# Kernel optimization log

Measured on AMD Instinct MI355X. Metric: run time of the kernel, lower is better.

Reference implementation:

```python
import jax, jax.numpy as jnp
import numpy as np
import math

DIM = 256
D_STATE = 16
D_CONV = 4
EXPAND = 2
D_INNER = EXPAND * DIM
DT_RANK = math.ceil(DIM / 16)
B_, H_, W_ = 2, 48, 48


def setup_inputs() -> dict:
    key = jax.random.key(0)
    ks = jax.random.split(key, 13)
    s = lambda *sh: 1.0 / np.sqrt(sh[-1])
    inp = {
        "x": jax.random.normal(ks[0], (B_, DIM, H_, W_), jnp.float32),
        "ln_w": jnp.ones((DIM,), jnp.float32),
        "ln_b": jnp.zeros((DIM,), jnp.float32),
        "in_proj_w": jax.random.normal(ks[1], (2 * D_INNER, DIM), jnp.float32) * s(DIM),
        "conv_w": jax.random.normal(ks[2], (D_INNER, 1, D_CONV), jnp.float32) * s(D_CONV),
        "conv_b": jax.random.normal(ks[3], (D_INNER,), jnp.float32) * 0.1,
        "x_proj_w": jax.random.normal(ks[4], (DT_RANK + 2 * D_STATE, D_INNER), jnp.float32) * s(D_INNER),
        "dt_proj_w": jax.random.normal(ks[5], (D_INNER, DT_RANK), jnp.float32) * s(DT_RANK),
        "dt_proj_b": jax.random.uniform(ks[6], (D_INNER,), jnp.float32, -4.0, -1.0),  # softplus -> small dt
        "A_log": jnp.log(jnp.broadcast_to(jnp.arange(1, D_STATE + 1, dtype=jnp.float32), (D_INNER, D_STATE))),
        "D": jnp.ones((D_INNER,), jnp.float32),
        "out_proj_w": jax.random.normal(ks[7], (DIM, D_INNER), jnp.float32) * s(D_INNER),
        "gamma": jax.random.normal(ks[8], (1,), jnp.float32) * 0.1,
    }
    return inp


def _mamba(seq, in_proj_w, conv_w, conv_b, x_proj_w, dt_proj_w, dt_proj_b, A_log, D, out_proj_w):
    # seq: [B, L, dim]
    B, L, _ = seq.shape
    xz = seq @ in_proj_w.T                       # [B, L, 2*d_inner]
    x_in, z = jnp.split(xz, 2, axis=-1)
    # depthwise causal conv over time
    xt = jnp.transpose(x_in, (0, 2, 1))          # [B, d_inner, L]
    xc = jax.lax.conv_general_dilated(
        xt, conv_w, window_strides=(1,), padding=[(D_CONV - 1, 0)],
        feature_group_count=D_INNER, dimension_numbers=("NCH", "OIH", "NCH"))
    xc = xc + conv_b[None, :, None]
    xc = jax.nn.silu(xc)
    xu = jnp.transpose(xc, (0, 2, 1))            # [B, L, d_inner]
    # input-dependent SSM params
    x_dbl = xu @ x_proj_w.T                      # [B, L, dt_rank + 2N]
    dt, Bm, Cm = jnp.split(x_dbl, [DT_RANK, DT_RANK + D_STATE], axis=-1)
    delta = jax.nn.softplus(dt @ dt_proj_w.T + dt_proj_b)   # [B, L, d_inner]
    A = -jnp.exp(A_log)                          # [d_inner, N]
    dA = jnp.exp(delta[..., None] * A)           # [B, L, d_inner, N]
    dBx = (delta * xu)[..., None] * Bm[:, :, None, :]        # [B, L, d_inner, N]

    def step(h, ins):
        dA_t, dBx_t, C_t = ins
        h = dA_t * h + dBx_t                     # [B, d_inner, N]
        y = jnp.einsum("bdn,bn->bd", h, C_t)
        return h, y

    h0 = jnp.zeros((B, D_INNER, D_STATE), seq.dtype)
    xs = (jnp.swapaxes(dA, 0, 1), jnp.swapaxes(dBx, 0, 1), jnp.swapaxes(Cm, 0, 1))
    _, ys = jax.lax.scan(step, h0, xs)           # ys: [L, B, d_inner]
    y = jnp.swapaxes(ys, 0, 1) + xu * D          # [B, L, d_inner]
    y = y * jax.nn.silu(z)
    return y @ out_proj_w.T                      # [B, L, dim]


def reference(x, ln_w, ln_b, in_proj_w, conv_w, conv_b, x_proj_w, dt_proj_w,
              dt_proj_b, A_log, D, out_proj_w, gamma):
    B, C, H, W = x.shape
    shortcut = x
    xp = jnp.transpose(x, (0, 2, 3, 1))          # [B, H, W, C]
    mu = jnp.mean(xp, axis=-1, keepdims=True)
    var = jnp.var(xp, axis=-1, keepdims=True)
    xn = (xp - mu) * jax.lax.rsqrt(var + 1e-5) * ln_w + ln_b
    seq = xn.reshape(B, H * W, C)
    y = _mamba(seq, in_proj_w, conv_w, conv_b, x_proj_w, dt_proj_w, dt_proj_b,
               A_log, D, out_proj_w)
    y = jnp.transpose(y.reshape(B, H, W, C), (0, 3, 1, 2))
    return shortcut + gamma * y
```

## Files before the change

### kernel.cpp

```cpp
#include <hip/hip_runtime.h>
#include <math.h>

#define DIMC 256
#define DST 16
#define DIN 512
#define BB 2
#define HH 48
#define WW 48
#define LL (HH*WW)
#define MM (BB*LL)
#define CH 12
#define NC 192
#define NGRP (BB*DIN)
#define NSEQ (NGRP*DST)
#define LTILE 16

typedef unsigned short ushort_t;
typedef __attribute__((ext_vector_type(8))) short bf16x8;
typedef __attribute__((ext_vector_type(4))) float f32x4;

__device__ __forceinline__ float silu_f(float a){ return a / (1.f + expf(-a)); }
__device__ __forceinline__ float softplus_f(float a){ return a > 20.f ? a : log1pf(__expf(a)); }
__device__ __forceinline__ ushort_t f2bf(float f) {
    unsigned u = __float_as_uint(f);
    u += 0x7FFFu + ((u >> 16) & 1u);
    return (ushort_t)(u >> 16);
}
__device__ __forceinline__ float bf2f(ushort_t h) {
    return __uint_as_float(((unsigned)h) << 16);
}

__global__ __launch_bounds__(256) void ln_kernel(const float* __restrict__ x,
    const float* __restrict__ w, const float* __restrict__ bgain,
    ushort_t* __restrict__ xn) {
    __shared__ float T2[LTILE][DIMC + 4];
    __shared__ float PS[16][17], PS2[16][17];
    __shared__ float MUB[LTILE], RB[LTILE];
    int blk = blockIdx.x;
    int b = blk / (LL/LTILE);
    int l0 = (blk % (LL/LTILE)) * LTILE;
    int t = threadIdx.x;
    int p = t & 15, g = t >> 4;
    float v[16];
    float s = 0.f, s2 = 0.f;
    #pragma unroll
    for (int cc = 0; cc < 16; cc++) {
        int c = g*16 + cc;
        float vv = x[((size_t)(b*DIMC + c))*LL + l0 + p];
        v[cc] = vv;
        s += vv; s2 += vv*vv;
    }
    PS[g][p] = s; PS2[g][p] = s2;
    __syncthreads();
    if (t < 16) {
        float tot = 0.f, tot2 = 0.f;
        #pragma unroll
        for (int gg = 0; gg < 16; gg++) { tot += PS[gg][t]; tot2 += PS2[gg][t]; }
        float mu = tot * (1.f/DIMC);
        float var = tot2 * (1.f/DIMC) - mu*mu;
        MUB[t] = mu;
        RB[t] = rsqrtf(var + 1e-5f);
    }
    __syncthreads();
    float mu = MUB[p], r = RB[p];
    #pragma unroll
    for (int cc = 0; cc < 16; cc++) {
        int c = g*16 + cc;
        T2[p][c] = (v[cc] - mu) * r * w[c] + bgain[c];
    }
    __syncthreads();
    int c4 = (t & 63) * 4;
    int prow = t >> 6;
    #pragma unroll
    for (int pp = 0; pp < 4; pp++) {
        int pos = pp*4 + prow;
        float4 q = *(const float4*)&T2[pos][c4];
        ushort4 o;
        o.x = f2bf(q.x); o.y = f2bf(q.y); o.z = f2bf(q.z); o.w = f2bf(q.w);
        *(ushort4*)&xn[((size_t)(b*LL + l0 + pos))*DIMC + c4] = o;
    }
}

#define W0N (1024*256)
#define W1N (48*512)
#define W2N (256*512)
__global__ __launch_bounds__(256) void wsetup_kernel(const float* __restrict__ w0,
    const float* __restrict__ w1, const float* __restrict__ w2,
    const float* __restrict__ A_log,
    ushort_t* __restrict__ o0, ushort_t* __restrict__ o1, ushort_t* __restrict__ o2,
    float* __restrict__ A2) {
    int i = blockIdx.x * 256 + threadIdx.x;
    if (i < W0N) o0[i] = f2bf(w0[i]);
    else if (i < W0N + W1N) o1[i - W0N] = f2bf(w1[i - W0N]);
    else if (i < W0N + W1N + W2N) o2[i - W0N - W1N] = f2bf(w2[i - W0N - W1N]);
    if (i < DIN*DST) A2[i] = -__expf(A_log[i]);
}

__global__ __launch_bounds__(256) void mfma_gemm128_split(const ushort_t* __restrict__ A,
    const ushort_t* __restrict__ W, ushort_t* __restrict__ Xs, float* __restrict__ Zb,
    int K) {
    __shared__ ushort_t Asl[128][72];
    __shared__ ushort_t Bsl[128][72];
    int tid = threadIdx.x;
    int bm = blockIdx.y * 128;
    int bn = blockIdx.x * 128;
    int w = tid >> 6, l = tid & 63;
    int wr = (w >> 1) * 64, wc = (w & 1) * 64;
    int fr = l & 15, fg = l >> 4;
    f32x4 acc[4][4] = {};
    for (int k0 = 0; k0 < K; k0 += 64) {
        #pragma unroll
        for (int s = 0; s < 4; s++) {
            int c = tid + s*256;
            int r = c >> 3, c8 = (c & 7) * 8;
            *(uint4*)&Asl[r][c8] = *(const uint4*)(A + (size_t)(bm + r)*K + k0 + c8);
            *(uint4*)&Bsl[r][c8] = *(const uint4*)(W + (size_t)(bn + r)*K + k0 + c8);
        }
        __syncthreads();
        #pragma unroll
        for (int kk = 0; kk < 2; kk++) {
            int ko = kk*32 + fg*8;
            bf16x8 af[4], bf[4];
            #pragma unroll
            for (int i = 0; i < 4; i++) af[i] = *(const bf16x8*)&Asl[wr + i*16 + fr][ko];
            #pragma unroll
            for (int j = 0; j < 4; j++) bf[j] = *(const bf16x8*)&Bsl[wc + j*16 + fr][ko];
            #pragma unroll
            for (int i = 0; i < 4; i++)
                #pragma unroll
                for (int j = 0; j < 4; j++)
                    acc[i][j] = __builtin_amdgcn_mfma_f32_16x16x32_bf16(af[i], bf[j], acc[i][j], 0,0,0);
        }
        __syncthreads();
    }
    #pragma unroll
    for (int i = 0; i < 4; i++)
        #pragma unroll
        for (int j = 0; j < 4; j++) {
            int n = bn + wc + j*16 + fr;
            int mbase = bm + wr + i*16 + fg*4;
            if (n < DIN) {
                #pragma unroll
                for (int ii = 0; ii < 4; ii++)
                    Xs[(size_t)(mbase+ii)*DIN + n] = f2bf(acc[i][j][ii]);
            } else {
                #pragma unroll
                for (int ii = 0; ii < 4; ii++)
                    Zb[(size_t)(mbase+ii)*DIN + (n - DIN)] = acc[i][j][ii];
            }
        }
}

template<int EPI>
__global__ __launch_bounds__(256) void mfma_gemm(const ushort_t* __restrict__ A,
    const ushort_t* __restrict__ W, float* __restrict__ C, int M, int N, int K,
    const float* __restrict__ Xres, const float* __restrict__ gammap,
    float* __restrict__ Out) {
    __shared__ ushort_t Asl[64][72];
    __shared__ ushort_t Bsl[64][72];
    int tid = threadIdx.x;
    int bm = blockIdx.y * 64;
    int bn = blockIdx.x * 64;
    int w = tid >> 6, l = tid & 63;
    int wr = (w >> 1) * 32, wc = (w & 1) * 32;
    int fr = l & 15, fg = l >> 4;
    f32x4 acc[2][2] = {};
    for (int k0 = 0; k0 < K; k0 += 64) {
        #pragma unroll
        for (int s = 0; s < 2; s++) {
            int c = tid + s*256;
            int r = c >> 3, c8 = (c & 7) * 8;
            *(uint4*)&Asl[r][c8] = *(const uint4*)(A + (size_t)(bm + r)*K + k0 + c8);
            uint4 wv = make_uint4(0u,0u,0u,0u);
            if (bn + r < N) wv = *(const uint4*)(W + (size_t)(bn + r)*K + k0 + c8);
            *(uint4*)&Bsl[r][c8] = wv;
        }
        __syncthreads();
        #pragma unroll
        for (int kk = 0; kk < 2; kk++) {
            int ko = kk*32 + fg*8;
            bf16x8 a0 = *(const bf16x8*)&Asl[wr + fr][ko];
            bf16x8 a1 = *(const bf16x8*)&Asl[wr + 16 + fr][ko];
            bf16x8 b0 = *(const bf16x8*)&Bsl[wc + fr][ko];
            bf16x8 b1 = *(const bf16x8*)&Bsl[wc + 16 + fr][ko];
            acc[0][0] = __builtin_amdgcn_mfma_f32_16x16x32_bf16(a0, b0, acc[0][0], 0,0,0);
            acc[0][1] = __builtin_amdgcn_mfma_f32_16x16x32_bf16(a0, b1, acc[0][1], 0,0,0);
            acc[1][0] = __builtin_amdgcn_mfma_f32_16x16x32_bf16(a1, b0, acc[1][0], 0,0,0);
            acc[1][1] = __builtin_amdgcn_mfma_f32_16x16x32_bf16(a1, b1, acc[1][1], 0,0,0);
        }
        __syncthreads();
    }
    if (EPI == 0) {
        #pragma unroll
        for (int mi = 0; mi < 2; mi++)
            #pragma unroll
            for (int nj = 0; nj < 2; nj++) {
                int n = bn + wc + nj*16 + fr;
                if (n < N) {
                    int mbase = bm + wr + mi*16 + fg*4;
                    #pragma unroll
                    for (int i = 0; i < 4; i++)
                        C[(size_t)(mbase + i)*N + n] = acc[mi][nj][i];
                }
            }
    } else {
        float g = gammap[0];
        int b = (bm >= LL) ? 1 : 0;
        #pragma unroll
        for (int mi = 0; mi < 2; mi++)
            #pragma unroll
            for (int nj = 0; nj < 2; nj++) {
                int n = bn + wc + nj*16 + fr;
                int mbase = bm + wr + mi*16 + fg*4;
                #pragma unroll
                for (int i = 0; i < 4; i++) {
                    size_t o = ((size_t)(b*DIMC + n))*LL + (size_t)(mbase + i - b*LL);
                    Out[o] = fmaf(g, acc[mi][nj][i], Xres[o]);
                }
            }
    }
}

__global__ __launch_bounds__(256) void conv_kernel(const ushort_t* __restrict__ xs,
    const float* __restrict__ cw, const float* __restrict__ cb,
    ushort_t* __restrict__ xu) {
    int idx = blockIdx.x * 256 + threadIdx.x;
    int d = idx & (DIN-1);
    int ml = idx >> 9;
    int l = ml % LL;
    float acc = cb[d];
    #pragma unroll
    for (int j = 0; j < 4; j++) {
        int ll = l - 3 + j;
        if (ll >= 0) acc = fmaf(cw[d*4 + j], bf2f(xs[(size_t)(ml - l + ll)*DIN + d]), acc);
    }
    xu[(size_t)ml*DIN + d] = f2bf(silu_f(acc));
}

#define LOAD16(arr, p) { float4 q0=(p)[0],q1=(p)[1],q2=(p)[2],q3=(p)[3]; \
    arr[0]=q0.x;arr[1]=q0.y;arr[2]=q0.z;arr[3]=q0.w; arr[4]=q1.x;arr[5]=q1.y;arr[6]=q1.z;arr[7]=q1.w; \
    arr[8]=q2.x;arr[9]=q2.y;arr[10]=q2.z;arr[11]=q2.w; arr[12]=q3.x;arr[13]=q3.y;arr[14]=q3.z;arr[15]=q3.w; }

#define DT_DOT(dlt, xr) { float4 t0 = (xr)[0], t1 = (xr)[1], t2 = (xr)[2], t3 = (xr)[3]; \
    dlt=fmaf(t0.x,dw[0],dlt); dlt=fmaf(t0.y,dw[1],dlt); dlt=fmaf(t0.z,dw[2],dlt); dlt=fmaf(t0.w,dw[3],dlt); \
    dlt=fmaf(t1.x,dw[4],dlt); dlt=fmaf(t1.y,dw[5],dlt); dlt=fmaf(t1.z,dw[6],dlt); dlt=fmaf(t1.w,dw[7],dlt); \
    dlt=fmaf(t2.x,dw[8],dlt); dlt=fmaf(t2.y,dw[9],dlt); dlt=fmaf(t2.z,dw[10],dlt); dlt=fmaf(t2.w,dw[11],dlt); \
    dlt=fmaf(t3.x,dw[12],dlt); dlt=fmaf(t3.y,dw[13],dlt); dlt=fmaf(t3.z,dw[14],dlt); dlt=fmaf(t3.w,dw[15],dlt); }

__global__ __launch_bounds__(256) void scan_phase1(
    const ushort_t* __restrict__ xu, const float* __restrict__ xdbl,
    const float* __restrict__ dtw, const float* __restrict__ dtb,
    const float* __restrict__ A2,
    float* __restrict__ aprod, float* __restrict__ hend) {
    __shared__ float xs_s[CH*48];
    int t = blockIdx.x * 256 + threadIdx.x;
    int g = t & (NGRP-1);
    int c = t >> 10;
    int b = g >> 9, d = g & (DIN-1);
    int m0 = b*LL + c*CH;
    for (int i = threadIdx.x; i < CH*48; i += 256) xs_s[i] = xdbl[(size_t)m0*48 + i];
    float dw[16], A[16], h[16], a[16];
    LOAD16(dw, (const float4*)(dtw + (size_t)d*16));
    LOAD16(A,  (const float4*)(A2  + (size_t)d*16));
    #pragma unroll
    for (int n = 0; n < 16; n++) { h[n] = 0.f; a[n] = 1.f; }
    float bias = dtb[d];
    __syncthreads();
    for (int l = 0; l < CH; l++) {
        const float4* xr = (const float4*)&xs_s[l*48];
        float dlt = bias;
        DT_DOT(dlt, xr);
        dlt = softplus_f(dlt);
        float xv = bf2f(xu[(size_t)(m0 + l)*DIN + d]);
        float dbx = dlt * xv;
        float Bv[16];
        LOAD16(Bv, xr + 4);
        #pragma unroll
        for (int n = 0; n < 16; n++) {
            float dA = __expf(dlt * A[n]);
            h[n] = fmaf(dA, h[n], dbx * Bv[n]);
            a[n] *= dA;
        }
    }
    float4* ap = (float4*)(aprod + ((size_t)c*NGRP + g)*16);
    float4* hp = (float4*)(hend  + ((size_t)c*NGRP + g)*16);
    ap[0] = make_float4(a[0],a[1],a[2],a[3]);   ap[1] = make_float4(a[4],a[5],a[6],a[7]);
    ap[2] = make_float4(a[8],a[9],a[10],a[11]); ap[3] = make_float4(a[12],a[13],a[14],a[15]);
    hp[0] = make_float4(h[0],h[1],h[2],h[3]);   hp[1] = make_float4(h[4],h[5],h[6],h[7]);
    hp[2] = make_float4(h[8],h[9],h[10],h[11]); hp[3] = make_float4(h[12],h[13],h[14],h[15]);
}

__global__ __launch_bounds__(256) void scan_phase2(const float* __restrict__ aprod,
    const float* __restrict__ hend, float* __restrict__ hin) {
    int u = blockIdx.x * 256 + threadIdx.x;
    float h = 0.f;
    #pragma unroll 4
    for (int c = 0; c < NC; c++) {
        size_t ci = (size_t)c*NSEQ + u;
        hin[ci] = h;
        h = fmaf(aprod[ci], h, hend[ci]);
    }
}

__global__ __launch_bounds__(256) void scan_phase3(
    const ushort_t* __restrict__ xu, const float* __restrict__ xdbl,
    const float* __restrict__ dtw, const float* __restrict__ dtb,
    const float* __restrict__ A2, const float* __restrict__ Dp,
    const float* __restrict__ zbuf, const float* __restrict__ hin,
    ushort_t* __restrict__ yg) {
    __shared__ float xs_s[CH*48];
    int t = blockIdx.x * 256 + threadIdx.x;
    int g = t & (NGRP-1);
    int c = t >> 10;
    int b = g >> 9, d = g & (DIN-1);
    int m0 = b*LL + c*CH;
    for (int i = threadIdx.x; i < CH*48; i += 256) xs_s[i] = xdbl[(size_t)m0*48 + i];
    float dw[16], A[16], h[16];
    LOAD16(dw, (const float4*)(dtw + (size_t)d*16));
    LOAD16(A,  (const float4*)(A2  + (size_t)d*16));
    LOAD16(h,  (const float4*)(hin + ((size_t)c*NGRP + g)*16));
    float bias = dtb[d];
    float Dd = Dp[d];
    __syncthreads();
    for (int l = 0; l < CH; l++) {
        int m = m0 + l;
        const float4* xr = (const float4*)&xs_s[l*48];
        float dlt = bias;
        DT_DOT(dlt, xr);
        dlt = softplus_f(dlt);
        float xv = bf2f(xu[(size_t)m*DIN + d]);
        float dbx = dlt * xv;
        float Bv[16], Cv[16];
        LOAD16(Bv, xr + 4);
        LOAD16(Cv, xr + 8);
        float y = 0.f;
        #pragma unroll
        for (int n = 0; n < 16; n++) {
            float dA = __expf(dlt * A[n]);
            h[n] = fmaf(dA, h[n], dbx * Bv[n]);
            y = fmaf(h[n], Cv[n], y);
        }
        float z = zbuf[(size_t)m*DIN + d];
        float yv = fmaf(xv, Dd, y);
        yg[(size_t)m*DIN + d] = f2bf(yv * (z / (1.f + __expf(-z))));
    }
}

extern "C" void kernel_launch(void* const* d_in, const int* in_sizes, int n_in,
                              void* d_out, int out_size, void* d_ws, size_t ws_size,
                              hipStream_t stream) {
    const float* x         = (const float*)d_in[0];
    const float* ln_w      = (const float*)d_in[1];
    const float* ln_b      = (const float*)d_in[2];
    const float* in_proj_w = (const float*)d_in[3];
    const float* conv_w    = (const float*)d_in[4];
    const float* conv_b    = (const float*)d_in[5];
    const float* x_proj_w  = (const float*)d_in[6];
    const float* dt_proj_w = (const float*)d_in[7];
    const float* dt_proj_b = (const float*)d_in[8];
    const float* A_log     = (const float*)d_in[9];
    const float* Dp        = (const float*)d_in[10];
    const float* out_proj_w= (const float*)d_in[11];
    const float* gamma     = (const float*)d_in[12];
    float* out = (float*)d_out;

    float* ws = (float*)d_ws;
    float* zbuf  = ws;
    float* x_dbl = zbuf  + (size_t)MM*DIN;
    float* aprod = x_dbl + (size_t)MM*48;
    float* hend  = aprod + (size_t)NC*NSEQ;
    float* hin   = hend  + (size_t)NC*NSEQ;
    float* A2    = hin   + (size_t)NC*NSEQ;
    ushort_t* xn  = (ushort_t*)(A2 + DIN*DST);
    ushort_t* xs  = xn  + (size_t)MM*DIMC;
    ushort_t* xu  = xs  + (size_t)MM*DIN;
    ushort_t* yg  = xu  + (size_t)MM*DIN;
    ushort_t* win = yg  + (size_t)MM*DIN;
    ushort_t* wxp = win + (size_t)W0N;
    ushort_t* wout= wxp + (size_t)W1N;

    ln_kernel<<<BB*(LL/LTILE), 256, 0, stream>>>(x, ln_w, ln_b, xn);
    wsetup_kernel<<<(W0N+W1N+W2N+255)/256, 256, 0, stream>>>(in_proj_w, x_proj_w, out_proj_w, A_log, win, wxp, wout, A2);
    mfma_gemm128_split<<<dim3(1024/128, MM/128), 256, 0, stream>>>(xn, win, xs, zbuf, DIMC);
    conv_kernel<<<(MM*DIN)/256, 256, 0, stream>>>(xs, conv_w, conv_b, xu);
    mfma_gemm<0><<<dim3(1, MM/64), 256, 0, stream>>>(xu, wxp, x_dbl, MM, 48, DIN, nullptr, nullptr, nullptr);
    scan_phase1<<<(NC*NGRP)/256, 256, 0, stream>>>(xu, x_dbl, dt_proj_w, dt_proj_b, A2, aprod, hend);
    scan_phase2<<<NSEQ/256, 256, 0, stream>>>(aprod, hend, hin);
    scan_phase3<<<(NC*NGRP)/256, 256, 0, stream>>>(xu, x_dbl, dt_proj_w, dt_proj_b, A2, Dp, zbuf, hin, yg);
    mfma_gemm<2><<<dim3(DIMC/64, MM/64), 256, 0, stream>>>(yg, wout, nullptr, MM, DIMC, DIN, x, gamma, out);
}
```

Baseline: 202.5 us.

## Fuse conv into x_proj GEMM, merge LN with weight setup, store z as bf16

Merges the layernorm and weight-conversion kernels into one launch. The depthwise causal conv plus SiLU now runs inside the x_proj GEMM tile loader, so a separate conv kernel is gone. The z half of in_proj is stored as bf16 instead of fp32, halving its write and read traffic. The cost is recomputing 3 halo rows per tile and some extra rounding on z. It also saves two kernel launches.

```diff
diff --git a/kernel.cpp b/kernel.cpp
--- a/kernel.cpp
+++ b/kernel.cpp
@@ -14,6 +14,11 @@
 #define NGRP (BB*DIN)
 #define NSEQ (NGRP*DST)
 #define LTILE 16
+#define NBLN (BB*(LL/LTILE))
+#define W0N (1024*256)
+#define W1N (48*512)
+#define W2N (256*512)
+#define NBW  ((W0N+W1N+W2N)/256)
 
 typedef unsigned short ushort_t;
 typedef __attribute__((ext_vector_type(8))) short bf16x8;
@@ -30,16 +35,27 @@
     return __uint_as_float(((unsigned)h) << 16);
 }
 
-__global__ __launch_bounds__(256) void ln_kernel(const float* __restrict__ x,
-    const float* __restrict__ w, const float* __restrict__ bgain,
-    ushort_t* __restrict__ xn) {
+__global__ __launch_bounds__(256) void prep_kernel(const float* __restrict__ x,
+    const float* __restrict__ w, const float* __restrict__ bgain, ushort_t* __restrict__ xn,
+    const float* __restrict__ w0, const float* __restrict__ w1, const float* __restrict__ w2,
+    const float* __restrict__ A_log,
+    ushort_t* __restrict__ o0, ushort_t* __restrict__ o1, ushort_t* __restrict__ o2,
+    float* __restrict__ A2) {
     __shared__ float T2[LTILE][DIMC + 4];
     __shared__ float PS[16][17], PS2[16][17];
     __shared__ float MUB[LTILE], RB[LTILE];
     int blk = blockIdx.x;
+    int t = threadIdx.x;
+    if (blk >= NBLN) {
+        int i = (blk - NBLN) * 256 + t;
+        if (i < W0N) o0[i] = f2bf(w0[i]);
+        else if (i < W0N + W1N) o1[i - W0N] = f2bf(w1[i - W0N]);
+        else o2[i - W0N - W1N] = f2bf(w2[i - W0N - W1N]);
+        if (i < DIN*DST) A2[i] = -__expf(A_log[i]);
+        return;
+    }
     int b = blk / (LL/LTILE);
     int l0 = (blk % (LL/LTILE)) * LTILE;
-    int t = threadIdx.x;
     int p = t & 15, g = t >> 4;
     float v[16];
     float s = 0.f, s2 = 0.f;
@@ -81,23 +97,8 @@
     }
 }
 
-#define W0N (1024*256)
-#define W1N (48*512)
-#define W2N (256*512)
-__global__ __launch_bounds__(256) void wsetup_kernel(const float* __restrict__ w0,
-    const float* __restrict__ w1, const float* __restrict__ w2,
-    const float* __restrict__ A_log,
-    ushort_t* __restrict__ o0, ushort_t* __restrict__ o1, ushort_t* __restrict__ o2,
-    float* __restrict__ A2) {
-    int i = blockIdx.x * 256 + threadIdx.x;
-    if (i < W0N) o0[i] = f2bf(w0[i]);
-    else if (i < W0N + W1N) o1[i - W0N] = f2bf(w1[i - W0N]);
-    else if (i < W0N + W1N + W2N) o2[i - W0N - W1N] = f2bf(w2[i - W0N - W1N]);
-    if (i < DIN*DST) A2[i] = -__expf(A_log[i]);
-}
-
 __global__ __launch_bounds__(256) void mfma_gemm128_split(const ushort_t* __restrict__ A,
-    const ushort_t* __restrict__ W, ushort_t* __restrict__ Xs, float* __restrict__ Zb,
+    const ushort_t* __restrict__ W, ushort_t* __restrict__ Xs, ushort_t* __restrict__ Zb,
     int K) {
     __shared__ ushort_t Asl[128][72];
     __shared__ ushort_t Bsl[128][72];
@@ -120,16 +121,16 @@
         #pragma unroll
         for (int kk = 0; kk < 2; kk++) {
             int ko = kk*32 + fg*8;
-            bf16x8 af[4], bf[4];
+            bf16x8 af[4], bfm[4];
             #pragma unroll
             for (int i = 0; i < 4; i++) af[i] = *(const bf16x8*)&Asl[wr + i*16 + fr][ko];
             #pragma unroll
-            for (int j = 0; j < 4; j++) bf[j] = *(const bf16x8*)&Bsl[wc + j*16 + fr][ko];
+            for (int j = 0; j < 4; j++) bfm[j] = *(const bf16x8*)&Bsl[wc + j*16 + fr][ko];
             #pragma unroll
             for (int i = 0; i < 4; i++)
                 #pragma unroll
                 for (int j = 0; j < 4; j++)
-                    acc[i][j] = __builtin_amdgcn_mfma_f32_16x16x32_bf16(af[i], bf[j], acc[i][j], 0,0,0);
+                    acc[i][j] = __builtin_amdgcn_mfma_f32_16x16x32_bf16(af[i], bfm[j], acc[i][j], 0,0,0);
         }
         __syncthreads();
     }
@@ -146,7 +147,84 @@
             } else {
                 #pragma unroll
                 for (int ii = 0; ii < 4; ii++)
-                    Zb[(size_t)(mbase+ii)*DIN + (n - DIN)] = acc[i][j][ii];
+                    Zb[(size_t)(mbase+ii)*DIN + (n - DIN)] = f2bf(acc[i][j][ii]);
+            }
+        }
+}
+
+__global__ __launch_bounds__(256) void xproj_conv_kernel(
+    const ushort_t* __restrict__ xs, const ushort_t* __restrict__ wxp,
+    const float* __restrict__ cw, const float* __restrict__ cb,
+    ushort_t* __restrict__ xu, float* __restrict__ xdbl) {
+    __shared__ ushort_t Xt[67][72];
+    __shared__ ushort_t As[64][72];
+    __shared__ ushort_t Bs[64][72];
+    int tid = threadIdx.x;
+    int R0 = blockIdx.x * 64;
+    int lmin = (R0 >= LL) ? LL : 0;
+    int w = tid >> 6, l = tid & 63;
+    int wr = (w >> 1) * 32, wc = (w & 1) * 32;
+    int fr = l & 15, fg = l >> 4;
+    f32x4 acc[2][2] = {};
+    for (int k0 = 0; k0 < DIN; k0 += 64) {
+        for (int i = tid; i < 67*8; i += 256) {
+            int r = i >> 3, c8 = (i & 7) * 8;
+            int m = R0 - 3 + r;
+            uint4 v = make_uint4(0u,0u,0u,0u);
+            if (m >= lmin) v = *(const uint4*)(xs + (size_t)m*DIN + k0 + c8);
+            *(uint4*)&Xt[r][c8] = v;
+        }
+        for (int i = tid; i < 64*8; i += 256) {
+            int r = i >> 3, c8 = (i & 7) * 8;
+            uint4 v = make_uint4(0u,0u,0u,0u);
+            if (r < 48) v = *(const uint4*)(wxp + (size_t)r*DIN + k0 + c8);
+            *(uint4*)&Bs[r][c8] = v;
+        }
+        __syncthreads();
+        #pragma unroll
+        for (int rr = 0; rr < 2; rr++) {
+            int r = (tid >> 3) + rr*32;
+            int c0 = (tid & 7) * 8;
+            ushort_t ov[8];
+            #pragma unroll
+            for (int cc = 0; cc < 8; cc++) {
+                int c = c0 + cc;
+                float4 cwv = ((const float4*)cw)[k0 + c];
+                float a = cb[k0 + c];
+                a = fmaf(cwv.x, bf2f(Xt[r+0][c]), a);
+                a = fmaf(cwv.y, bf2f(Xt[r+1][c]), a);
+                a = fmaf(cwv.z, bf2f(Xt[r+2][c]), a);
+                a = fmaf(cwv.w, bf2f(Xt[r+3][c]), a);
+                ov[cc] = f2bf(silu_f(a));
+            }
+            *(uint4*)&As[r][c0] = *(uint4*)ov;
+            *(uint4*)(xu + (size_t)(R0 + r)*DIN + k0 + c0) = *(uint4*)ov;
+        }
+        __syncthreads();
+        #pragma unroll
+        for (int kk = 0; kk < 2; kk++) {
+            int ko = kk*32 + fg*8;
+            bf16x8 a0 = *(const bf16x8*)&As[wr + fr][ko];
+            bf16x8 a1 = *(const bf16x8*)&As[wr + 16 + fr][ko];
+            bf16x8 b0 = *(const bf16x8*)&Bs[wc + fr][ko];
+            bf16x8 b1 = *(const bf16x8*)&Bs[wc + 16 + fr][ko];
+            acc[0][0] = __builtin_amdgcn_mfma_f32_16x16x32_bf16(a0, b0, acc[0][0], 0,0,0);
+            acc[0][1] = __builtin_amdgcn_mfma_f32_16x16x32_bf16(a0, b1, acc[0][1], 0,0,0);
+            acc[1][0] = __builtin_amdgcn_mfma_f32_16x16x32_bf16(a1, b0, acc[1][0], 0,0,0);
+            acc[1][1] = __builtin_amdgcn_mfma_f32_16x16x32_bf16(a1, b1, acc[1][1], 0,0,0);
+        }
+        __syncthreads();
+    }
+    #pragma unroll
+    for (int mi = 0; mi < 2; mi++)
+        #pragma unroll
+        for (int nj = 0; nj < 2; nj++) {
+            int n = wc + nj*16 + fr;
+            if (n < 48) {
+                int mbase = R0 + wr + mi*16 + fg*4;
+                #pragma unroll
+                for (int i = 0; i < 4; i++)
+                    xdbl[(size_t)(mbase + i)*48 + n] = acc[mi][nj][i];
             }
         }
 }
@@ -221,22 +299,6 @@
     }
 }
 
-__global__ __launch_bounds__(256) void conv_kernel(const ushort_t* __restrict__ xs,
-    const float* __restrict__ cw, const float* __restrict__ cb,
-    ushort_t* __restrict__ xu) {
-    int idx = blockIdx.x * 256 + threadIdx.x;
-    int d = idx & (DIN-1);
-    int ml = idx >> 9;
-    int l = ml % LL;
-    float acc = cb[d];
-    #pragma unroll
-    for (int j = 0; j < 4; j++) {
-        int ll = l - 3 + j;
-        if (ll >= 0) acc = fmaf(cw[d*4 + j], bf2f(xs[(size_t)(ml - l + ll)*DIN + d]), acc);
-    }
-    xu[(size_t)ml*DIN + d] = f2bf(silu_f(acc));
-}
-
 #define LOAD16(arr, p) { float4 q0=(p)[0],q1=(p)[1],q2=(p)[2],q3=(p)[3]; \
     arr[0]=q0.x;arr[1]=q0.y;arr[2]=q0.z;arr[3]=q0.w; arr[4]=q1.x;arr[5]=q1.y;arr[6]=q1.z;arr[7]=q1.w; \
     arr[8]=q2.x;arr[9]=q2.y;arr[10]=q2.z;arr[11]=q2.w; arr[12]=q3.x;arr[13]=q3.y;arr[14]=q3.z;arr[15]=q3.w; }
@@ -306,7 +368,7 @@
     const ushort_t* __restrict__ xu, const float* __restrict__ xdbl,
     const float* __restrict__ dtw, const float* __restrict__ dtb,
     const float* __restrict__ A2, const float* __restrict__ Dp,
-    const float* __restrict__ zbuf, const float* __restrict__ hin,
+    const ushort_t* __restrict__ zb, const float* __restrict__ hin,
     ushort_t* __restrict__ yg) {
     __shared__ float xs_s[CH*48];
     int t = blockIdx.x * 256 + threadIdx.x;
@@ -340,7 +402,7 @@
             h[n] = fmaf(dA, h[n], dbx * Bv[n]);
             y = fmaf(h[n], Cv[n], y);
         }
-        float z = zbuf[(size_t)m*DIN + d];
+        float z = bf2f(zb[(size_t)m*DIN + d]);
         float yv = fmaf(xv, Dd, y);
         yg[(size_t)m*DIN + d] = f2bf(yv * (z / (1.f + __expf(-z))));
     }
@@ -365,27 +427,26 @@
     float* out = (float*)d_out;
 
     float* ws = (float*)d_ws;
-    float* zbuf  = ws;
-    float* x_dbl = zbuf  + (size_t)MM*DIN;
+    float* x_dbl = ws;
     float* aprod = x_dbl + (size_t)MM*48;
     float* hend  = aprod + (size_t)NC*NSEQ;
     float* hin   = hend  + (size_t)NC*NSEQ;
     float* A2    = hin   + (size_t)NC*NSEQ;
     ushort_t* xn  = (ushort_t*)(A2 + DIN*DST);
     ushort_t* xs  = xn  + (size_t)MM*DIMC;
-    ushort_t* xu  = xs  + (size_t)MM*DIN;
+    ushort_t* zb  = xs  + (size_t)MM*DIN;
+    ushort_t* xu  = zb  + (size_t)MM*DIN;
     ushort_t* yg  = xu  + (size_t)MM*DIN;
     ushort_t* win = yg  + (size_t)MM*DIN;
     ushort_t* wxp = win + (size_t)W0N;
     ushort_t* wout= wxp + (size_t)W1N;
 
-    ln_kernel<<<BB*(LL/LTILE), 256, 0, stream>>>(x, ln_w, ln_b, xn);
-    wsetup_kernel<<<(W0N+W1N+W2N+255)/256, 256, 0, stream>>>(in_proj_w, x_proj_w, out_proj_w, A_log, win, wxp, wout, A2);
-    mfma_gemm128_split<<<dim3(1024/128, MM/128), 256, 0, stream>>>(xn, win, xs, zbuf, DIMC);
-    conv_kernel<<<(MM*DIN)/256, 256, 0, stream>>>(xs, conv_w, conv_b, xu);
-    mfma_gemm<0><<<dim3(1, MM/64), 256, 0, stream>>>(xu, wxp, x_dbl, MM, 48, DIN, nullptr, nullptr, nullptr);
+    prep_kernel<<<NBLN + NBW, 256, 0, stream>>>(x, ln_w, ln_b, xn,
+        in_proj_w, x_proj_w, out_proj_w, A_log, win, wxp, wout, A2);
+    mfma_gemm128_split<<<dim3(1024/128, MM/128), 256, 0, stream>>>(xn, win, xs, zb, DIMC);
+    xproj_conv_kernel<<<MM/64, 256, 0, stream>>>(xs, wxp, conv_w, conv_b, xu, x_dbl);
     scan_phase1<<<(NC*NGRP)/256, 256, 0, stream>>>(xu, x_dbl, dt_proj_w, dt_proj_b, A2, aprod, hend);
     scan_phase2<<<NSEQ/256, 256, 0, stream>>>(aprod, hend, hin);
-    scan_phase3<<<(NC*NGRP)/256, 256, 0, stream>>>(xu, x_dbl, dt_proj_w, dt_proj_b, A2, Dp, zbuf, hin, yg);
+    scan_phase3<<<(NC*NGRP)/256, 256, 0, stream>>>(xu, x_dbl, dt_proj_w, dt_proj_b, A2, Dp, zb, hin, yg);
     mfma_gemm<2><<<dim3(DIMC/64, MM/64), 256, 0, stream>>>(yg, wout, nullptr, MM, DIMC, DIN, x, gamma, out);
 }
```

Result: slower. 209.4 us (+3.4%).

## Fuse scan phases into a cooperative kernel, merge prep kernels, store z in bf16

Applied to the files above, without the earlier changes.

Three scan kernels become one cooperative kernel that uses two grid-wide syncs in place of separate launches, and it keeps the phase-1 registers alive into phase 3. The chunk length is doubled, so there are half as many chunks. Layernorm and weight conversion are merged into one prep kernel that converts with float4 loads, and the z gate buffer is stored as bf16 instead of fp32 to cut memory traffic. The cooperative launch needs all 384 blocks resident at once. The serial cross-chunk scan uses only NSEQ threads while the rest of the grid waits, and bf16 z adds rounding error.

```diff
diff --git a/kernel.cpp b/kernel.cpp
--- a/kernel.cpp
+++ b/kernel.cpp
@@ -1,5 +1,8 @@
 #include <hip/hip_runtime.h>
+#include <hip/hip_cooperative_groups.h>
 #include <math.h>
+
+namespace cg = cooperative_groups;
 
 #define DIMC 256
 #define DST 16
@@ -9,11 +12,16 @@
 #define WW 48
 #define LL (HH*WW)
 #define MM (BB*LL)
-#define CH 12
-#define NC 192
+#define CH 24
+#define NC 96
 #define NGRP (BB*DIN)
 #define NSEQ (NGRP*DST)
 #define LTILE 16
+#define NBLN (BB*(LL/LTILE))
+#define W0N (1024*256)
+#define W1N (48*512)
+#define W2N (256*512)
+#define NB4  ((W0N+W1N+W2N)/4/256)
 
 typedef unsigned short ushort_t;
 typedef __attribute__((ext_vector_type(8))) short bf16x8;
@@ -30,16 +38,36 @@
     return __uint_as_float(((unsigned)h) << 16);
 }
 
-__global__ __launch_bounds__(256) void ln_kernel(const float* __restrict__ x,
-    const float* __restrict__ w, const float* __restrict__ bgain,
-    ushort_t* __restrict__ xn) {
+__global__ __launch_bounds__(256) void prep_kernel(const float* __restrict__ x,
+    const float* __restrict__ w, const float* __restrict__ bgain, ushort_t* __restrict__ xn,
+    const float* __restrict__ w0, const float* __restrict__ w1, const float* __restrict__ w2,
+    const float* __restrict__ A_log,
+    ushort_t* __restrict__ o0, ushort_t* __restrict__ o1, ushort_t* __restrict__ o2,
+    float* __restrict__ A2) {
     __shared__ float T2[LTILE][DIMC + 4];
     __shared__ float PS[16][17], PS2[16][17];
     __shared__ float MUB[LTILE], RB[LTILE];
     int blk = blockIdx.x;
+    int t = threadIdx.x;
+    if (blk >= NBLN) {
+        int i = (blk - NBLN) * 256 + t;
+        if (i < 2048) {
+            float4 q = ((const float4*)A_log)[i];
+            float4 o = make_float4(-__expf(q.x), -__expf(q.y), -__expf(q.z), -__expf(q.w));
+            ((float4*)A2)[i] = o;
+        }
+        const float* src; ushort_t* dst; int j;
+        if (i < W0N/4) { src = w0; dst = o0; j = i; }
+        else if (i < (W0N+W1N)/4) { src = w1; dst = o1; j = i - W0N/4; }
+        else { src = w2; dst = o2; j = i - (W0N+W1N)/4; }
+        float4 q = ((const float4*)src)[j];
+        ushort4 u;
+        u.x = f2bf(q.x); u.y = f2bf(q.y); u.z = f2bf(q.z); u.w = f2bf(q.w);
+        ((ushort4*)dst)[j] = u;
+        return;
+    }
     int b = blk / (LL/LTILE);
     int l0 = (blk % (LL/LTILE)) * LTILE;
-    int t = threadIdx.x;
     int p = t & 15, g = t >> 4;
     float v[16];
     float s = 0.f, s2 = 0.f;
@@ -81,23 +109,8 @@
     }
 }
 
-#define W0N (1024*256)
-#define W1N (48*512)
-#define W2N (256*512)
-__global__ __launch_bounds__(256) void wsetup_kernel(const float* __restrict__ w0,
-    const float* __restrict__ w1, const float* __restrict__ w2,
-    const float* __restrict__ A_log,
-    ushort_t* __restrict__ o0, ushort_t* __restrict__ o1, ushort_t* __restrict__ o2,
-    float* __restrict__ A2) {
-    int i = blockIdx.x * 256 + threadIdx.x;
-    if (i < W0N) o0[i] = f2bf(w0[i]);
-    else if (i < W0N + W1N) o1[i - W0N] = f2bf(w1[i - W0N]);
-    else if (i < W0N + W1N + W2N) o2[i - W0N - W1N] = f2bf(w2[i - W0N - W1N]);
-    if (i < DIN*DST) A2[i] = -__expf(A_log[i]);
-}
-
 __global__ __launch_bounds__(256) void mfma_gemm128_split(const ushort_t* __restrict__ A,
-    const ushort_t* __restrict__ W, ushort_t* __restrict__ Xs, float* __restrict__ Zb,
+    const ushort_t* __restrict__ W, ushort_t* __restrict__ Xs, ushort_t* __restrict__ Zb,
     int K) {
     __shared__ ushort_t Asl[128][72];
     __shared__ ushort_t Bsl[128][72];
@@ -120,16 +133,16 @@
         #pragma unroll
         for (int kk = 0; kk < 2; kk++) {
             int ko = kk*32 + fg*8;
-            bf16x8 af[4], bf[4];
+            bf16x8 af[4], bfm[4];
             #pragma unroll
             for (int i = 0; i < 4; i++) af[i] = *(const bf16x8*)&Asl[wr + i*16 + fr][ko];
             #pragma unroll
-            for (int j = 0; j < 4; j++) bf[j] = *(const bf16x8*)&Bsl[wc + j*16 + fr][ko];
+            for (int j = 0; j < 4; j++) bfm[j] = *(const bf16x8*)&Bsl[wc + j*16 + fr][ko];
             #pragma unroll
             for (int i = 0; i < 4; i++)
                 #pragma unroll
                 for (int j = 0; j < 4; j++)
-                    acc[i][j] = __builtin_amdgcn_mfma_f32_16x16x32_bf16(af[i], bf[j], acc[i][j], 0,0,0);
+                    acc[i][j] = __builtin_amdgcn_mfma_f32_16x16x32_bf16(af[i], bfm[j], acc[i][j], 0,0,0);
         }
         __syncthreads();
     }
@@ -146,9 +159,25 @@
             } else {
                 #pragma unroll
                 for (int ii = 0; ii < 4; ii++)
-                    Zb[(size_t)(mbase+ii)*DIN + (n - DIN)] = acc[i][j][ii];
+                    Zb[(size_t)(mbase+ii)*DIN + (n - DIN)] = f2bf(acc[i][j][ii]);
             }
         }
+}
+
+__global__ __launch_bounds__(256) void conv_kernel(const ushort_t* __restrict__ xs,
+    const float* __restrict__ cw, const float* __restrict__ cb,
+    ushort_t* __restrict__ xu) {
+    int idx = blockIdx.x * 256 + threadIdx.x;
+    int d = idx & (DIN-1);
+    int ml = idx >> 9;
+    int l = ml % LL;
+    float acc = cb[d];
+    #pragma unroll
+    for (int j = 0; j < 4; j++) {
+        int ll = l - 3 + j;
+        if (ll >= 0) acc = fmaf(cw[d*4 + j], bf2f(xs[(size_t)(ml - l + ll)*DIN + d]), acc);
+    }
+    xu[(size_t)ml*DIN + d] = f2bf(silu_f(acc));
 }
 
 template<int EPI>
@@ -221,22 +250,6 @@
     }
 }
 
-__global__ __launch_bounds__(256) void conv_kernel(const ushort_t* __restrict__ xs,
-    const float* __restrict__ cw, const float* __restrict__ cb,
-    ushort_t* __restrict__ xu) {
-    int idx = blockIdx.x * 256 + threadIdx.x;
-    int d = idx & (DIN-1);
-    int ml = idx >> 9;
-    int l = ml % LL;
-    float acc = cb[d];
-    #pragma unroll
-    for (int j = 0; j < 4; j++) {
-        int ll = l - 3 + j;
-        if (ll >= 0) acc = fmaf(cw[d*4 + j], bf2f(xs[(size_t)(ml - l + ll)*DIN + d]), acc);
-    }
-    xu[(size_t)ml*DIN + d] = f2bf(silu_f(acc));
-}
-
 #define LOAD16(arr, p) { float4 q0=(p)[0],q1=(p)[1],q2=(p)[2],q3=(p)[3]; \
     arr[0]=q0.x;arr[1]=q0.y;arr[2]=q0.z;arr[3]=q0.w; arr[4]=q1.x;arr[5]=q1.y;arr[6]=q1.z;arr[7]=q1.w; \
     arr[8]=q2.x;arr[9]=q2.y;arr[10]=q2.z;arr[11]=q2.w; arr[12]=q3.x;arr[13]=q3.y;arr[14]=q3.z;arr[15]=q3.w; }
@@ -247,11 +260,14 @@
     dlt=fmaf(t2.x,dw[8],dlt); dlt=fmaf(t2.y,dw[9],dlt); dlt=fmaf(t2.z,dw[10],dlt); dlt=fmaf(t2.w,dw[11],dlt); \
     dlt=fmaf(t3.x,dw[12],dlt); dlt=fmaf(t3.y,dw[13],dlt); dlt=fmaf(t3.z,dw[14],dlt); dlt=fmaf(t3.w,dw[15],dlt); }
 
-__global__ __launch_bounds__(256) void scan_phase1(
+__global__ __launch_bounds__(256) void scan_coop(
     const ushort_t* __restrict__ xu, const float* __restrict__ xdbl,
     const float* __restrict__ dtw, const float* __restrict__ dtb,
-    const float* __restrict__ A2,
-    float* __restrict__ aprod, float* __restrict__ hend) {
+    const float* __restrict__ A2, const float* __restrict__ Dp,
+    const ushort_t* __restrict__ zb,
+    float* __restrict__ aprod, float* __restrict__ hend, float* __restrict__ hin,
+    ushort_t* __restrict__ yg) {
+    cg::grid_group grid = cg::this_grid();
     __shared__ float xs_s[CH*48];
     int t = blockIdx.x * 256 + threadIdx.x;
     int g = t & (NGRP-1);
@@ -282,46 +298,27 @@
             a[n] *= dA;
         }
     }
-    float4* ap = (float4*)(aprod + ((size_t)c*NGRP + g)*16);
-    float4* hp = (float4*)(hend  + ((size_t)c*NGRP + g)*16);
-    ap[0] = make_float4(a[0],a[1],a[2],a[3]);   ap[1] = make_float4(a[4],a[5],a[6],a[7]);
-    ap[2] = make_float4(a[8],a[9],a[10],a[11]); ap[3] = make_float4(a[12],a[13],a[14],a[15]);
-    hp[0] = make_float4(h[0],h[1],h[2],h[3]);   hp[1] = make_float4(h[4],h[5],h[6],h[7]);
-    hp[2] = make_float4(h[8],h[9],h[10],h[11]); hp[3] = make_float4(h[12],h[13],h[14],h[15]);
-}
-
-__global__ __launch_bounds__(256) void scan_phase2(const float* __restrict__ aprod,
-    const float* __restrict__ hend, float* __restrict__ hin) {
-    int u = blockIdx.x * 256 + threadIdx.x;
-    float h = 0.f;
-    #pragma unroll 4
-    for (int c = 0; c < NC; c++) {
-        size_t ci = (size_t)c*NSEQ + u;
-        hin[ci] = h;
-        h = fmaf(aprod[ci], h, hend[ci]);
-    }
-}
-
-__global__ __launch_bounds__(256) void scan_phase3(
-    const ushort_t* __restrict__ xu, const float* __restrict__ xdbl,
-    const float* __restrict__ dtw, const float* __restrict__ dtb,
-    const float* __restrict__ A2, const float* __restrict__ Dp,
-    const float* __restrict__ zbuf, const float* __restrict__ hin,
-    ushort_t* __restrict__ yg) {
-    __shared__ float xs_s[CH*48];
-    int t = blockIdx.x * 256 + threadIdx.x;
-    int g = t & (NGRP-1);
-    int c = t >> 10;
-    int b = g >> 9, d = g & (DIN-1);
-    int m0 = b*LL + c*CH;
-    for (int i = threadIdx.x; i < CH*48; i += 256) xs_s[i] = xdbl[(size_t)m0*48 + i];
-    float dw[16], A[16], h[16];
-    LOAD16(dw, (const float4*)(dtw + (size_t)d*16));
-    LOAD16(A,  (const float4*)(A2  + (size_t)d*16));
-    LOAD16(h,  (const float4*)(hin + ((size_t)c*NGRP + g)*16));
-    float bias = dtb[d];
+    {
+        float4* ap = (float4*)(aprod + ((size_t)c*NGRP + g)*16);
+        float4* hp = (float4*)(hend  + ((size_t)c*NGRP + g)*16);
+        ap[0] = make_float4(a[0],a[1],a[2],a[3]);   ap[1] = make_float4(a[4],a[5],a[6],a[7]);
+        ap[2] = make_float4(a[8],a[9],a[10],a[11]); ap[3] = make_float4(a[12],a[13],a[14],a[15]);
+        hp[0] = make_float4(h[0],h[1],h[2],h[3]);   hp[1] = make_float4(h[4],h[5],h[6],h[7]);
+        hp[2] = make_float4(h[8],h[9],h[10],h[11]); hp[3] = make_float4(h[12],h[13],h[14],h[15]);
+    }
+    grid.sync();
+    if (t < NSEQ) {
+        float hh = 0.f;
+        #pragma unroll 4
+        for (int cc = 0; cc < NC; cc++) {
+            size_t ci = (size_t)cc*NSEQ + t;
+            hin[ci] = hh;
+            hh = fmaf(aprod[ci], hh, hend[ci]);
+        }
+    }
+    grid.sync();
+    LOAD16(h, (const float4*)(hin + ((size_t)c*NGRP + g)*16));
     float Dd = Dp[d];
-    __syncthreads();
     for (int l = 0; l < CH; l++) {
         int m = m0 + l;
         const float4* xr = (const float4*)&xs_s[l*48];
@@ -340,7 +337,7 @@
             h[n] = fmaf(dA, h[n], dbx * Bv[n]);
             y = fmaf(h[n], Cv[n], y);
         }
-        float z = zbuf[(size_t)m*DIN + d];
+        float z = bf2f(zb[(size_t)m*DIN + d]);
         float yv = fmaf(xv, Dd, y);
         yg[(size_t)m*DIN + d] = f2bf(yv * (z / (1.f + __expf(-z))));
     }
@@ -365,27 +362,35 @@
     float* out = (float*)d_out;
 
     float* ws = (float*)d_ws;
-    float* zbuf  = ws;
-    float* x_dbl = zbuf  + (size_t)MM*DIN;
+    float* x_dbl = ws;
     float* aprod = x_dbl + (size_t)MM*48;
     float* hend  = aprod + (size_t)NC*NSEQ;
     float* hin   = hend  + (size_t)NC*NSEQ;
     float* A2    = hin   + (size_t)NC*NSEQ;
     ushort_t* xn  = (ushort_t*)(A2 + DIN*DST);
     ushort_t* xs  = xn  + (size_t)MM*DIMC;
-    ushort_t* xu  = xs  + (size_t)MM*DIN;
+    ushort_t* zb  = xs  + (size_t)MM*DIN;
+    ushort_t* xu  = zb  + (size_t)MM*DIN;
     ushort_t* yg  = xu  + (size_t)MM*DIN;
     ushort_t* win = yg  + (size_t)MM*DIN;
     ushort_t* wxp = win + (size_t)W0N;
     ushort_t* wout= wxp + (size_t)W1N;
 
-    ln_kernel<<<BB*(LL/LTILE), 256, 0, stream>>>(x, ln_w, ln_b, xn);
-    wsetup_kernel<<<(W0N+W1N+W2N+255)/256, 256, 0, stream>>>(in_proj_w, x_proj_w, out_proj_w, A_log, win, wxp, wout, A2);
-    mfma_gemm128_split<<<dim3(1024/128, MM/128), 256, 0, stream>>>(xn, win, xs, zbuf, DIMC);
+    prep_kernel<<<NBLN + NB4, 256, 0, stream>>>(x, ln_w, ln_b, xn,
+        in_proj_w, x_proj_w, out_proj_w, A_log, win, wxp, wout, A2);
+    mfma_gemm128_split<<<dim3(1024/128, MM/128), 256, 0, stream>>>(xn, win, xs, zb, DIMC);
     conv_kernel<<<(MM*DIN)/256, 256, 0, stream>>>(xs, conv_w, conv_b, xu);
     mfma_gemm<0><<<dim3(1, MM/64), 256, 0, stream>>>(xu, wxp, x_dbl, MM, 48, DIN, nullptr, nullptr, nullptr);
-    scan_phase1<<<(NC*NGRP)/256, 256, 0, stream>>>(xu, x_dbl, dt_proj_w, dt_proj_b, A2, aprod, hend);
-    scan_phase2<<<NSEQ/256, 256, 0, stream>>>(aprod, hend, hin);
-    scan_phase3<<<(NC*NGRP)/256, 256, 0, stream>>>(xu, x_dbl, dt_proj_w, dt_proj_b, A2, Dp, zbuf, hin, yg);
+    {
+        const ushort_t* xu_c = xu;  const float* xdbl_c = x_dbl;
+        const float* dtw_c = dt_proj_w; const float* dtb_c = dt_proj_b;
+        const float* A2_c = A2; const float* Dp_c = Dp; const ushort_t* zb_c = zb;
+        float* ap = aprod; float* he = hend; float* hi = hin; ushort_t* yg_c = yg;
+        void* args[] = { (void*)&xu_c, (void*)&xdbl_c, (void*)&dtw_c, (void*)&dtb_c,
+                         (void*)&A2_c, (void*)&Dp_c, (void*)&zb_c,
+                         (void*)&ap, (void*)&he, (void*)&hi, (void*)&yg_c };
+        hipLaunchCooperativeKernel((void*)scan_coop, dim3((NC*NGRP)/256), dim3(256),
+                                   args, 0, stream);
+    }
     mfma_gemm<2><<<dim3(DIMC/64, MM/64), 256, 0, stream>>>(yg, wout, nullptr, MM, DIMC, DIN, x, gamma, out);
 }
```

Measured after the change: 322.5 us. +59.3%, slower.
